# Kernel tuning notes

Measured on AMD Instinct MI355X. Metric: run time of the kernel, lower is better.

The kernel has to match this reference:

```python
import jax, jax.numpy as jnp
import numpy as np

NUM_CLASSES = 6
EPS = 1e-10


def setup_inputs() -> dict:
    key = jax.random.key(0)
    k1, k2 = jax.random.split(key)
    latent = jax.random.normal(k1, (8192, 128), dtype=jnp.float32)
    label = jax.random.randint(k2, (8192,), 0, NUM_CLASSES, dtype=jnp.int64)
    return {"latent": latent, "label": label}


def reference(latent, label):
    # Full pairwise cosine similarity: S[a,b] = <x_a, x_b> / max(|x_a||x_b|, eps)
    # (matches torch.nn.CosineSimilarity's per-pair clamped denominator)
    norms = jnp.linalg.norm(latent, axis=1)                      # [B]
    dots = latent @ latent.T                                      # [B, B]
    S = dots / jnp.maximum(norms[:, None] * norms[None, :], EPS)  # [B, B]

    # Per-class-pair block sums: P[i,j] = sum_{a in class i, b in class j} S[a,b]
    onehot = jax.nn.one_hot(label, NUM_CLASSES, dtype=latent.dtype)  # [B, C]
    P = onehot.T @ S @ onehot                                        # [C, C]
    counts = jnp.sum(onehot, axis=0)                                 # [C]

    # Original divides block (i,j) by max(1, n_i^2 - n_i) (uses first class's size)
    denom = jnp.maximum(counts * counts - counts, 1.0)               # [C]
    iu, ju = jnp.triu_indices(NUM_CLASSES, k=1)
    dists = P[iu, ju] / denom[iu]
    return jnp.mean(dists)
```

## Files before the change

### kernel.cpp

```cpp
#include <hip/hip_runtime.h>

#define BATCH 8192
#define DIM 128
#define NCLS 6
#define NPAIRS 15
#define NBLK 128
#define NTHR 512
#define WPB (NTHR / 64)
#define NWAVES (NBLK * WPB)
#define RPW (BATCH / NWAVES)
#define ITERS (RPW / 2)
#define ZLEN (NCLS * DIM)
#define NTHR2 832


__global__ __launch_bounds__(NTHR) void class_sum_kernel(
    const float* __restrict__ latent,
    const int* __restrict__ label,
    float* __restrict__ gpart,
    float* __restrict__ gcntp)
{
    __shared__ float lz[WPB][ZLEN];
    __shared__ int   lcnt[WPB][NCLS];

    const int tid  = threadIdx.x;
    const int lane = tid & 63;
    const int w    = tid >> 6;
    const int half = lane >> 5;
    const int hl   = lane & 31;
    const int gw   = blockIdx.x * WPB + w;
    const int row0 = gw * RPW + half;

    const float* bp = latent + (size_t)row0 * DIM + hl * 4;
    float4 v[ITERS];
    int labs[ITERS];
    #pragma unroll
    for (int j = 0; j < ITERS; ++j)
        v[j] = *reinterpret_cast<const float4*>(bp + (size_t)j * 2 * DIM);
    #pragma unroll
    for (int j = 0; j < ITERS; ++j)
        labs[j] = label[row0 + 2 * j];

    float4 acc[NCLS];
    int    cnt[NCLS];
    #pragma unroll
    for (int c = 0; c < NCLS; ++c) { acc[c] = make_float4(0.f, 0.f, 0.f, 0.f); cnt[c] = 0; }

    #pragma unroll
    for (int j = 0; j < ITERS; ++j) {
        float ss = v[j].x * v[j].x + v[j].y * v[j].y
                 + v[j].z * v[j].z + v[j].w * v[j].w;
        #pragma unroll
        for (int off = 16; off >= 1; off >>= 1)
            ss += __shfl_xor(ss, off);
        const float rn = 1.0f / sqrtf(ss);
        const int lab = labs[j];
        #pragma unroll
        for (int c = 0; c < NCLS; ++c) {
            const float m = (lab == c) ? rn : 0.0f;
            acc[c].x += v[j].x * m;  acc[c].y += v[j].y * m;
            acc[c].z += v[j].z * m;  acc[c].w += v[j].w * m;
            cnt[c]   += (hl == 0) ? (int)(lab == c) : 0;
        }
    }

    #pragma unroll
    for (int c = 0; c < NCLS; ++c) {
        acc[c].x += __shfl_xor(acc[c].x, 32);
        acc[c].y += __shfl_xor(acc[c].y, 32);
        acc[c].z += __shfl_xor(acc[c].z, 32);
        acc[c].w += __shfl_xor(acc[c].w, 32);
        cnt[c]   += __shfl_xor(cnt[c], 32);
    }

    if (lane < 32) {
        #pragma unroll
        for (int c = 0; c < NCLS; ++c)
            *reinterpret_cast<float4*>(&lz[w][c * DIM + lane * 4]) = acc[c];
    }
    if (lane == 0) {
        #pragma unroll
        for (int c = 0; c < NCLS; ++c) lcnt[w][c] = cnt[c];
    }
    __syncthreads();

    for (int e = tid; e < ZLEN; e += NTHR) {
        float s = 0.f;
        #pragma unroll
        for (int ww = 0; ww < WPB; ++ww) s += lz[ww][e];
        gpart[blockIdx.x * ZLEN + e] = s;
    }
    if (tid < NCLS) {
        int s = 0;
        #pragma unroll
        for (int ww = 0; ww < WPB; ++ww) s += lcnt[ww][tid];
        gcntp[blockIdx.x * NCLS + tid] = (float)s;
    }
}

__global__ __launch_bounds__(NTHR2) void finalize_kernel(
    const float* __restrict__ gpart,
    const float* __restrict__ gcntp,
    float* __restrict__ out)
{
    __shared__ float zz[ZLEN];
    __shared__ float cf[NCLS];
    __shared__ float ps[NPAIRS];
    const int tid = threadIdx.x;

    if (tid < ZLEN) {
        float s = 0.f;
        #pragma unroll 16
        for (int b = 0; b < NBLK; ++b) s += gpart[b * ZLEN + tid];
        zz[tid] = s;
    } else if (tid < ZLEN + NCLS) {
        const int c = tid - ZLEN;
        float s = 0.f;
        #pragma unroll 16
        for (int b = 0; b < NBLK; ++b) s += gcntp[b * NCLS + c];
        cf[c] = s;
    }
    if (tid >= NTHR2 - NPAIRS) ps[tid - (NTHR2 - NPAIRS)] = 0.f;
    __syncthreads();

    if (tid < DIM) {
        float zi[NCLS];
        #pragma unroll
        for (int c = 0; c < NCLS; ++c) zi[c] = zz[c * DIM + tid];
        int p = 0;
        #pragma unroll
        for (int i = 0; i < NCLS; ++i) {
            #pragma unroll
            for (int j = i + 1; j < NCLS; ++j, ++p)
                atomicAdd(&ps[p], zi[i] * zi[j]);
        }
    }
    __syncthreads();

    if (tid == 0) {
        float acc2 = 0.f;
        int p = 0;
        for (int i = 0; i < NCLS; ++i) {
            const float n = cf[i];
            const float denom = fmaxf(n * n - n, 1.0f);
            for (int j = i + 1; j < NCLS; ++j, ++p)
                acc2 += ps[p] / denom;
        }
        out[0] = acc2 / (float)NPAIRS;
    }
}

extern "C" void kernel_launch(void* const* d_in, const int* in_sizes, int n_in,
                              void* d_out, int out_size, void* d_ws, size_t ws_size,
                              hipStream_t stream) {
    const float* latent = (const float*)d_in[0];
    const int* label = (const int*)d_in[1];
    float* out = (float*)d_out;

    float* gpart = (float*)d_ws;
    float* gcntp = gpart + NBLK * ZLEN;

    class_sum_kernel<<<NBLK, NTHR, 0, stream>>>(latent, label, gpart, gcntp);
    finalize_kernel<<<1, NTHR2, 0, stream>>>(gpart, gcntp, out);
}
```

Baseline: 44.05 us.

## Fuse class-sum and finalize kernels with flag-based grid synchronization

Merges the two kernel launches into a single kernel: every block publishes its partial class sums and then sets a release flag, and block 0 spins on all flags before doing the final reduction and pairwise dot products. It also halves the block count and doubles the threads per block. The aim is to drop the second launch and the gap between kernels. In exchange it depends on all 64 blocks being co-resident and on the workspace flags starting out not equal to the magic value, and block 0 now serializes the final work after a spin-wait.

```diff
diff --git a/kernel.cpp b/kernel.cpp
--- a/kernel.cpp
+++ b/kernel.cpp
@@ -4,21 +4,23 @@
 #define DIM 128
 #define NCLS 6
 #define NPAIRS 15
-#define NBLK 128
-#define NTHR 512
+#define NBLK 64
+#define NTHR 1024
 #define WPB (NTHR / 64)
 #define NWAVES (NBLK * WPB)
 #define RPW (BATCH / NWAVES)
 #define ITERS (RPW / 2)
 #define ZLEN (NCLS * DIM)
-#define NTHR2 832
+#define MAGIC 0x5CA1AB1Eu
 
 
-__global__ __launch_bounds__(NTHR) void class_sum_kernel(
+__global__ __launch_bounds__(NTHR) void fused_kernel(
     const float* __restrict__ latent,
     const int* __restrict__ label,
     float* __restrict__ gpart,
-    float* __restrict__ gcntp)
+    float* __restrict__ gcntp,
+    unsigned int* __restrict__ flags,
+    float* __restrict__ out)
 {
     __shared__ float lz[WPB][ZLEN];
     __shared__ int   lcnt[WPB][NCLS];
@@ -84,29 +86,40 @@
     }
     __syncthreads();
 
-    for (int e = tid; e < ZLEN; e += NTHR) {
+    if (tid < ZLEN) {
         float s = 0.f;
         #pragma unroll
-        for (int ww = 0; ww < WPB; ++ww) s += lz[ww][e];
-        gpart[blockIdx.x * ZLEN + e] = s;
-    }
-    if (tid < NCLS) {
+        for (int ww = 0; ww < WPB; ++ww) s += lz[ww][tid];
+        gpart[blockIdx.x * ZLEN + tid] = s;
+    } else if (tid < ZLEN + NCLS) {
+        const int c = tid - ZLEN;
         int s = 0;
         #pragma unroll
-        for (int ww = 0; ww < WPB; ++ww) s += lcnt[ww][tid];
-        gcntp[blockIdx.x * NCLS + tid] = (float)s;
+        for (int ww = 0; ww < WPB; ++ww) s += lcnt[ww][c];
+        gcntp[blockIdx.x * NCLS + c] = (float)s;
     }
-}
 
-__global__ __launch_bounds__(NTHR2) void finalize_kernel(
-    const float* __restrict__ gpart,
-    const float* __restrict__ gcntp,
-    float* __restrict__ out)
-{
+    __threadfence();
+    __syncthreads();
+    if (tid == 0)
+        __hip_atomic_store(&flags[blockIdx.x], MAGIC,
+                           __ATOMIC_RELEASE, __HIP_MEMORY_SCOPE_AGENT);
+
+    if (blockIdx.x != 0) return;
+
+    if (tid < NBLK) {
+        while (__hip_atomic_load(&flags[tid], __ATOMIC_ACQUIRE,
+                                 __HIP_MEMORY_SCOPE_AGENT) != MAGIC)
+            __builtin_amdgcn_s_sleep(1);
+        __hip_atomic_store(&flags[tid], 0u,
+                           __ATOMIC_RELAXED, __HIP_MEMORY_SCOPE_AGENT);
+    }
+    __syncthreads();
+    __threadfence();
+
     __shared__ float zz[ZLEN];
     __shared__ float cf[NCLS];
     __shared__ float ps[NPAIRS];
-    const int tid = threadIdx.x;
 
     if (tid < ZLEN) {
         float s = 0.f;
@@ -120,7 +133,7 @@
         for (int b = 0; b < NBLK; ++b) s += gcntp[b * NCLS + c];
         cf[c] = s;
     }
-    if (tid >= NTHR2 - NPAIRS) ps[tid - (NTHR2 - NPAIRS)] = 0.f;
+    if (tid >= NTHR - NPAIRS) ps[tid - (NTHR - NPAIRS)] = 0.f;
     __syncthreads();
 
     if (tid < DIM) {
@@ -159,7 +172,7 @@
 
     float* gpart = (float*)d_ws;
     float* gcntp = gpart + NBLK * ZLEN;
+    unsigned int* flags = (unsigned int*)(gcntp + NBLK * NCLS);
 
-    class_sum_kernel<<<NBLK, NTHR, 0, stream>>>(latent, label, gpart, gcntp);
-    finalize_kernel<<<1, NTHR2, 0, stream>>>(gpart, gcntp, out);
+    fused_kernel<<<NBLK, NTHR, 0, stream>>>(latent, label, gpart, gcntp, flags, out);
 }
```

After: 62.80 us. +42.6%, slower.
